# Kernel tuning notes

Measured on AMD Instinct MI355X. Metric: run time of the kernel, lower is better.

The kernel has to match this reference:

```python
import jax, jax.numpy as jnp
import numpy as np

INF = 1000000000000000.0  # 1e15, matches the TF source

B, H, S, D = 4, 16, 1024, 64


def setup_inputs() -> dict:
    key = jax.random.key(0)
    kq, kk, kv, kp = jax.random.split(key, 4)
    q = jax.random.normal(kq, (B, H, S, D), dtype=jnp.float32)
    k = jax.random.normal(kk, (B, H, S, D), dtype=jnp.float32)
    v = jax.random.normal(kv, (B, H, S, D), dtype=jnp.float32)
    # pad_mask: 1 = masked-out key position, broadcast over heads and queries
    pad_mask = jax.random.randint(kp, (B, 1, 1, S), 0, 2, dtype=jnp.int32)
    # look_ahead_mask: 1 above the diagonal (future positions masked)
    look_ahead_mask = jnp.triu(jnp.ones((S, S), dtype=jnp.int32), k=1)[None, None]
    return {"q": q, "k": k, "v": v, "pad_mask": pad_mask,
            "look_ahead_mask": look_ahead_mask}


def reference(q, k, v, pad_mask, look_ahead_mask):
    d_model = jnp.float32(q.shape[3])
    # scores: (B, H, Sq, Sk)
    score_logits = jnp.einsum("bhqd,bhkd->bhqk", q, k) / jnp.sqrt(d_model)
    if pad_mask is not None:
        score_logits = score_logits + pad_mask.astype(jnp.float32) * (-INF)
    if look_ahead_mask is not None:
        score_logits = score_logits + look_ahead_mask.astype(jnp.float32) * (-INF)
    attention_weights = jax.nn.softmax(score_logits, axis=-1)
    context_vector = jnp.einsum("bhqk,bhkd->bhqd", attention_weights, v)
    return (context_vector, attention_weights)
```

## Files before the change

kernel.cpp:

```cpp
#include <hip/hip_runtime.h>
#include <stdint.h>

#define S 1024
#define D 64
#define TQ 16
#define KT 128
#define NKT 8
#define NEG (-1e15f)
#define SCALE 0.125f

#define WB_STRIDE 1048
#define KB_STRIDE 72
#define VT_STRIDE 136
#define QS_STRIDE 72

typedef __bf16 bf16x8 __attribute__((ext_vector_type(8)));
typedef float f32x4 __attribute__((ext_vector_type(4)));
typedef unsigned short ushort_t;

__device__ __forceinline__ unsigned short f2b(float f) {
  union { float f; uint32_t u; } c; c.f = f;
  uint32_t u = c.u;
  return (unsigned short)((u + 0x7fffu + ((u >> 16) & 1u)) >> 16);
}
__device__ __forceinline__ float b2f(uint32_t u) {
  union { uint32_t u; float f; } c; c.u = u << 16;
  return c.f;
}

__device__ __forceinline__ void barrier_lds_only() {
  asm volatile("s_waitcnt lgkmcnt(0)" ::: "memory");
  __builtin_amdgcn_s_barrier();
  __builtin_amdgcn_sched_barrier(0);
}

__global__ __launch_bounds__(256) void prep_k_kernel(
    const float* __restrict__ Kg, ushort_t* __restrict__ Kb)
{
  const size_t idx = ((size_t)blockIdx.x * 256 + threadIdx.x) * 8;
  float4 a = *(const float4*)(Kg + idx);
  float4 b = *(const float4*)(Kg + idx + 4);
  ushort_t tmp[8];
  tmp[0]=f2b(a.x); tmp[1]=f2b(a.y); tmp[2]=f2b(a.z); tmp[3]=f2b(a.w);
  tmp[4]=f2b(b.x); tmp[5]=f2b(b.y); tmp[6]=f2b(b.z); tmp[7]=f2b(b.w);
  *(uint4*)(Kb + idx) = *(const uint4*)tmp;
}

__global__ __launch_bounds__(256) void prep_vt_kernel(
    const float* __restrict__ Vg, ushort_t* __restrict__ Vt)
{
  __shared__ __align__(16) ushort_t lvt[D * QS_STRIDE];
  const int t = threadIdx.x;
  const int bh = blockIdx.x >> 4;
  const int j0 = (blockIdx.x & 15) << 6;

  {
    const int j = t >> 2, sd = (t & 3) << 4;
    const float* src = Vg + ((size_t)bh * S + j0 + j) * D + sd;
#pragma unroll
    for (int c = 0; c < 4; ++c) {
      float4 f = *(const float4*)(src + (c << 2));
      lvt[(sd + (c << 2) + 0) * QS_STRIDE + j] = f2b(f.x);
      lvt[(sd + (c << 2) + 1) * QS_STRIDE + j] = f2b(f.y);
      lvt[(sd + (c << 2) + 2) * QS_STRIDE + j] = f2b(f.z);
      lvt[(sd + (c << 2) + 3) * QS_STRIDE + j] = f2b(f.w);
    }
  }
  __syncthreads();
  {
    const int d = t >> 2, sj = (t & 3) << 4;
    ushort_t tmp[16];
#pragma unroll
    for (int c = 0; c < 4; ++c)
      *(ushort4*)&tmp[c << 2] = *(const ushort4*)&lvt[d * QS_STRIDE + sj + (c << 2)];
    ushort_t* dst = Vt + ((size_t)bh * D + d) * S + j0 + sj;
    *(uint4*)dst = *(const uint4*)&tmp[0];
    *(uint4*)(dst + 8) = *(const uint4*)&tmp[8];
  }
}

__global__ __launch_bounds__(512, 6) void attn_kernel(
    const float* __restrict__ Qg, const ushort_t* __restrict__ Kb,
    const ushort_t* __restrict__ Vtb, const int* __restrict__ PADg,
    float* __restrict__ OCTX, float* __restrict__ OW)
{
  __shared__ __align__(16) ushort_t wb[TQ * WB_STRIDE];
  __shared__ __align__(16) ushort_t ub[KT * KB_STRIDE];

  const int t  = threadIdx.x;
  const int w  = t >> 6;
  const int l  = t & 63;
  const int la = l & 15;
  const int lb = l >> 4;

  const int hwblk = blockIdx.x;
  const int slot  = hwblk >> 3;
  const int bh    = ((hwblk & 7) << 3) + (slot >> 6);
  const int qt    = slot & 63;
  const int qr0   = qt << 4;

  const size_t head = (size_t)bh * S * D;
  const int* pp = PADg + (size_t)(bh >> 4) * S;

  bf16x8 aq0, aq1;
  {
    const float* qrow = Qg + head + (size_t)(qr0 + la) * D + (lb << 3);
    float4 q00 = *(const float4*)(qrow);
    float4 q01 = *(const float4*)(qrow + 4);
    float4 q10 = *(const float4*)(qrow + 32);
    float4 q11 = *(const float4*)(qrow + 36);
    ushort_t a0[8], a1[8];
    a0[0]=f2b(q00.x); a0[1]=f2b(q00.y); a0[2]=f2b(q00.z); a0[3]=f2b(q00.w);
    a0[4]=f2b(q01.x); a0[5]=f2b(q01.y); a0[6]=f2b(q01.z); a0[7]=f2b(q01.w);
    a1[0]=f2b(q10.x); a1[1]=f2b(q10.y); a1[2]=f2b(q10.z); a1[3]=f2b(q10.w);
    a1[4]=f2b(q11.x); a1[5]=f2b(q11.y); a1[6]=f2b(q11.z); a1[7]=f2b(q11.w);
    aq0 = *(const bf16x8*)a0;
    aq1 = *(const bf16x8*)a1;
  }

  {
    const int krow = t >> 2, koff = (t & 3) << 4;
    const ushort_t* ksrc = Kb + head + (size_t)krow * D + koff;
    ushort_t* kdst = &ub[krow * KB_STRIDE + koff];
    uint4 kra = *(const uint4*)(ksrc);
    uint4 krb = *(const uint4*)(ksrc + 8);
    for (int kt = 0; kt < NKT; ++kt) {
      *(uint4*)kdst = kra;
      *(uint4*)(kdst + 8) = krb;
      barrier_lds_only();
      if (kt + 1 < NKT) {
        const ushort_t* nsrc = ksrc + (size_t)(kt + 1) * (KT * D);
        kra = *(const uint4*)(nsrc);
        krb = *(const uint4*)(nsrc + 8);
      }
      const int j0 = w << 4;
      f32x4 acc = {0.f, 0.f, 0.f, 0.f};
      bf16x8 b0 = *(const bf16x8*)&ub[(j0 + la) * KB_STRIDE + (lb << 3)];
      acc = __builtin_amdgcn_mfma_f32_16x16x32_bf16(aq0, b0, acc, 0, 0, 0);
      bf16x8 b1 = *(const bf16x8*)&ub[(j0 + la) * KB_STRIDE + 32 + (lb << 3)];
      acc = __builtin_amdgcn_mfma_f32_16x16x32_bf16(aq1, b1, acc, 0, 0, 0);
#pragma unroll
      for (int i = 0; i < 4; ++i)
        wb[((lb << 2) + i) * WB_STRIDE + kt * KT + j0 + la] = f2b(acc[i]);
      barrier_lds_only();
    }
  }

  const int vrow = t >> 3, voff = (t & 7) << 4;
  const ushort_t* vsrc = Vtb + (size_t)bh * (D * S) + (size_t)vrow * S + voff;
  uint4 vra = *(const uint4*)(vsrc);
  uint4 vrb = *(const uint4*)(vsrc + 8);

#pragma unroll
  for (int rr = 0; rr < 2; ++rr) {
    const int r  = (w << 1) + rr;
    const int qr = qr0 + r;
    float lg[16];
    float m = -3.0e38f;
#pragma unroll
    for (int ii = 0; ii < 8; ++ii) {
      const int j = (l << 1) + (ii << 7);
      uint32_t pr = *(const uint32_t*)&wb[r * WB_STRIDE + j];
      int2 pv = *(const int2*)&pp[j];
      float l0 = b2f(pr & 0xffffu) * SCALE + (pv.x ? NEG : 0.0f) + ((j     > qr) ? NEG : 0.0f);
      float l1 = b2f(pr >> 16)     * SCALE + (pv.y ? NEG : 0.0f) + ((j + 1 > qr) ? NEG : 0.0f);
      lg[2 * ii] = l0; lg[2 * ii + 1] = l1;
      m = fmaxf(m, fmaxf(l0, l1));
    }
#pragma unroll
    for (int off = 32; off > 0; off >>= 1) m = fmaxf(m, __shfl_xor(m, off, 64));
    float sum = 0.f;
#pragma unroll
    for (int x = 0; x < 16; ++x) { lg[x] = __expf(lg[x] - m); sum += lg[x]; }
#pragma unroll
    for (int off = 32; off > 0; off >>= 1) sum += __shfl_xor(sum, off, 64);
    const float inv = 1.0f / sum;
    float* orow = OW + (size_t)(bh * S + qr) * S;
#pragma unroll
    for (int ii = 0; ii < 8; ++ii) {
      const int j = (l << 1) + (ii << 7);
      float w0 = lg[2 * ii] * inv, w1 = lg[2 * ii + 1] * inv;
      *(uint32_t*)&wb[r * WB_STRIDE + j] = ((uint32_t)f2b(w1) << 16) | (uint32_t)f2b(w0);
      unsigned long long uw = ((unsigned long long)__float_as_uint(w1) << 32)
                            | (unsigned long long)__float_as_uint(w0);
      __builtin_nontemporal_store(uw, (unsigned long long*)&orow[j]);
    }
  }
  barrier_lds_only();

  const int jh = w >> 2;
  const int d0 = (w & 3) << 4;
  ushort_t* vdst = &ub[vrow * VT_STRIDE + voff];
  f32x4 cacc = {0.f, 0.f, 0.f, 0.f};
  for (int kt = 0; kt < NKT; ++kt) {
    *(uint4*)vdst = vra;
    *(uint4*)(vdst + 8) = vrb;
    barrier_lds_only();
    if (kt + 1 < NKT) {
      const ushort_t* nv = vsrc + (kt + 1) * KT;
      vra = *(const uint4*)(nv);
      vrb = *(const uint4*)(nv + 8);
    }
#pragma unroll
    for (int ks = 0; ks < 2; ++ks) {
      const int jt = jh * 64 + ks * 32;
      bf16x8 af = *(const bf16x8*)&wb[la * WB_STRIDE + kt * KT + jt + (lb << 3)];
      bf16x8 bf = *(const bf16x8*)&ub[(d0 + la) * VT_STRIDE + jt + (lb << 3)];
      cacc = __builtin_amdgcn_mfma_f32_16x16x32_bf16(af, bf, cacc, 0, 0, 0);
    }
    barrier_lds_only();
  }

  float* pbuf = (float*)ub;
  if (w >= 4) {
#pragma unroll
    for (int i = 0; i < 4; ++i)
      pbuf[(w - 4) * 320 + ((lb << 2) + i) * 20 + la] = cacc[i];
  }
  barrier_lds_only();
  if (w < 4) {
#pragma unroll
    for (int i = 0; i < 4; ++i) {
      const int qrow = (lb << 2) + i;
      __builtin_nontemporal_store(
          cacc[i] + pbuf[w * 320 + qrow * 20 + la],
          &OCTX[((size_t)(bh * S) + qr0 + qrow) * D + d0 + la]);
    }
  }
}

extern "C" void kernel_launch(void* const* d_in, const int* in_sizes, int n_in,
                              void* d_out, int out_size, void* d_ws, size_t ws_size,
                              hipStream_t stream) {
  const float* q   = (const float*)d_in[0];
  const float* k   = (const float*)d_in[1];
  const float* v   = (const float*)d_in[2];
  const int*   pad = (const int*)d_in[3];
  float* ctx  = (float*)d_out;
  float* wout = (float*)d_out + (size_t)4 * 16 * S * D;

  ushort_t* Kb  = (ushort_t*)d_ws;
  ushort_t* Vtb = (ushort_t*)d_ws + (size_t)4 * 16 * S * D;

  prep_k_kernel <<<dim3(2048), dim3(256), 0, stream>>>(k, Kb);
  prep_vt_kernel<<<dim3(1024), dim3(256), 0, stream>>>(v, Vtb);
  attn_kernel   <<<dim3(4096), dim3(512), 0, stream>>>(q, Kb, Vtb, pad, ctx, wout);
}
```

Baseline: 390.4 us.

## Make K/V staging wave-private to drop per-tile barriers and prefetch two tiles

Each wave now loads exactly the K rows and V-transpose slice it later reads from LDS, so the per-tile workgroup barriers in the QK and PV loops are removed and only one barrier remains after each loop. Global loads are double-buffered two tiles ahead in registers and the loops are fully unrolled. This targets barrier stalls and global load latency, at the cost of more registers under a 512-thread, 6-block launch bound. It relies on the LDS write and read by the same wave being ordered without an explicit wait.

```diff
diff --git a/kernel.cpp b/kernel.cpp
--- a/kernel.cpp
+++ b/kernel.cpp
@@ -119,21 +119,26 @@
   }
 
   {
-    const int krow = t >> 2, koff = (t & 3) << 4;
-    const ushort_t* ksrc = Kb + head + (size_t)krow * D + koff;
-    ushort_t* kdst = &ub[krow * KB_STRIDE + koff];
-    uint4 kra = *(const uint4*)(ksrc);
-    uint4 krb = *(const uint4*)(ksrc + 8);
+    const int kr = l >> 2;
+    const int ko = (l & 3) << 4;
+    const int rowg = (w << 4) + kr;
+    const ushort_t* ksrc = Kb + head + (size_t)rowg * D + ko;
+    ushort_t* kdst = &ub[rowg * KB_STRIDE + ko];
+    const int j0 = w << 4;
+    uint4 kra[2], krb[2];
+    kra[0] = *(const uint4*)(ksrc);
+    krb[0] = *(const uint4*)(ksrc + 8);
+    kra[1] = *(const uint4*)(ksrc + (size_t)(KT * D));
+    krb[1] = *(const uint4*)(ksrc + (size_t)(KT * D) + 8);
+#pragma unroll
     for (int kt = 0; kt < NKT; ++kt) {
-      *(uint4*)kdst = kra;
-      *(uint4*)(kdst + 8) = krb;
-      barrier_lds_only();
-      if (kt + 1 < NKT) {
-        const ushort_t* nsrc = ksrc + (size_t)(kt + 1) * (KT * D);
-        kra = *(const uint4*)(nsrc);
-        krb = *(const uint4*)(nsrc + 8);
+      *(uint4*)kdst = kra[kt & 1];
+      *(uint4*)(kdst + 8) = krb[kt & 1];
+      if (kt + 2 < NKT) {
+        const ushort_t* ns = ksrc + (size_t)(kt + 2) * (KT * D);
+        kra[kt & 1] = *(const uint4*)(ns);
+        krb[kt & 1] = *(const uint4*)(ns + 8);
       }
-      const int j0 = w << 4;
       f32x4 acc = {0.f, 0.f, 0.f, 0.f};
       bf16x8 b0 = *(const bf16x8*)&ub[(j0 + la) * KB_STRIDE + (lb << 3)];
       acc = __builtin_amdgcn_mfma_f32_16x16x32_bf16(aq0, b0, acc, 0, 0, 0);
@@ -142,14 +147,22 @@
 #pragma unroll
       for (int i = 0; i < 4; ++i)
         wb[((lb << 2) + i) * WB_STRIDE + kt * KT + j0 + la] = f2b(acc[i]);
-      barrier_lds_only();
-    }
-  }
-
-  const int vrow = t >> 3, voff = (t & 7) << 4;
-  const ushort_t* vsrc = Vtb + (size_t)bh * (D * S) + (size_t)vrow * S + voff;
-  uint4 vra = *(const uint4*)(vsrc);
-  uint4 vrb = *(const uint4*)(vsrc + 8);
+    }
+  }
+  barrier_lds_only();
+
+  const int jh = w >> 2;
+  const int d0 = (w & 3) << 4;
+  const int vr = l >> 2;
+  const int vo = (l & 3) << 4;
+  const ushort_t* vsrc = Vtb + (size_t)bh * (D * S) + (size_t)(d0 + vr) * S
+                        + jh * 64 + vo;
+  ushort_t* vdst = &ub[(d0 + vr) * VT_STRIDE + jh * 64 + vo];
+  uint4 vra[2], vrb[2];
+  vra[0] = *(const uint4*)(vsrc);
+  vrb[0] = *(const uint4*)(vsrc + 8);
+  vra[1] = *(const uint4*)(vsrc + KT);
+  vrb[1] = *(const uint4*)(vsrc + KT + 8);
 
 #pragma unroll
   for (int rr = 0; rr < 2; ++rr) {
@@ -188,28 +201,27 @@
   }
   barrier_lds_only();
 
-  const int jh = w >> 2;
-  const int d0 = (w & 3) << 4;
-  ushort_t* vdst = &ub[vrow * VT_STRIDE + voff];
   f32x4 cacc = {0.f, 0.f, 0.f, 0.f};
-  for (int kt = 0; kt < NKT; ++kt) {
-    *(uint4*)vdst = vra;
-    *(uint4*)(vdst + 8) = vrb;
-    barrier_lds_only();
-    if (kt + 1 < NKT) {
-      const ushort_t* nv = vsrc + (kt + 1) * KT;
-      vra = *(const uint4*)(nv);
-      vrb = *(const uint4*)(nv + 8);
-    }
-#pragma unroll
-    for (int ks = 0; ks < 2; ++ks) {
-      const int jt = jh * 64 + ks * 32;
-      bf16x8 af = *(const bf16x8*)&wb[la * WB_STRIDE + kt * KT + jt + (lb << 3)];
-      bf16x8 bf = *(const bf16x8*)&ub[(d0 + la) * VT_STRIDE + jt + (lb << 3)];
-      cacc = __builtin_amdgcn_mfma_f32_16x16x32_bf16(af, bf, cacc, 0, 0, 0);
-    }
-    barrier_lds_only();
-  }
+  {
+#pragma unroll
+    for (int kt = 0; kt < NKT; ++kt) {
+      *(uint4*)vdst = vra[kt & 1];
+      *(uint4*)(vdst + 8) = vrb[kt & 1];
+      if (kt + 2 < NKT) {
+        const ushort_t* nv = vsrc + (kt + 2) * KT;
+        vra[kt & 1] = *(const uint4*)(nv);
+        vrb[kt & 1] = *(const uint4*)(nv + 8);
+      }
+#pragma unroll
+      for (int ks = 0; ks < 2; ++ks) {
+        const int jt = jh * 64 + ks * 32;
+        bf16x8 af = *(const bf16x8*)&wb[la * WB_STRIDE + kt * KT + jt + (lb << 3)];
+        bf16x8 bf = *(const bf16x8*)&ub[(d0 + la) * VT_STRIDE + jt + (lb << 3)];
+        cacc = __builtin_amdgcn_mfma_f32_16x16x32_bf16(af, bf, cacc, 0, 0, 0);
+      }
+    }
+  }
+  barrier_lds_only();
 
   float* pbuf = (float*)ub;
   if (w >= 4) {
```

After: 380.3 us. 2.6% less time.
